# Kernel tuning notes

Hardware: AMD Instinct MI355X
Metric: run time of the kernel (lower is better)

## Reference

```python
import jax, jax.numpy as jnp
import numpy as np

N = 20000      # nodes
E = 320000     # edges (avg degree 16)
F_IN = 32      # raw node feature dim
D = 128        # GNN_EMBEDDING_DIM = out_channels per head
HEADS = 4
RNN_H = 128    # RNN_HIDDEN_DIM
NEG_SLOPE = 0.2


def setup_inputs() -> dict:
    key = jax.random.key(0)
    ks = jax.random.split(key, 16)
    s = 0.05
    return {
        "node_features": jax.random.normal(ks[0], (N, F_IN), jnp.float32),
        "hidden_state": jax.random.normal(ks[1], (1, RNN_H), jnp.float32),
        "W_enc": jax.random.normal(ks[2], (F_IN, D), jnp.float32) * s,
        "b_enc": jax.random.normal(ks[3], (D,), jnp.float32) * s,
        "W_l": jax.random.normal(ks[4], (D, HEADS * D), jnp.float32) * s,
        "b_l": jax.random.normal(ks[5], (HEADS * D,), jnp.float32) * s,
        "W_r": jax.random.normal(ks[6], (D, HEADS * D), jnp.float32) * s,
        "b_r": jax.random.normal(ks[7], (HEADS * D,), jnp.float32) * s,
        "att": jax.random.normal(ks[8], (HEADS, D), jnp.float32) * s,
        "gat_bias": jax.random.normal(ks[9], (D,), jnp.float32) * s,
        "W_ih": jax.random.normal(ks[10], (3 * RNN_H, D), jnp.float32) * s,
        "W_hh": jax.random.normal(ks[11], (3 * RNN_H, RNN_H), jnp.float32) * s,
        "b_ih": jax.random.normal(ks[12], (3 * RNN_H,), jnp.float32) * s,
        "b_hh": jax.random.normal(ks[13], (3 * RNN_H,), jnp.float32) * s,
        "edge_index": jax.random.randint(ks[14], (2, E), 0, N, jnp.int32),
    }


def reference(node_features, hidden_state, W_enc, b_enc, W_l, b_l, W_r, b_r,
              att, gat_bias, W_ih, W_hh, b_ih, b_hh, edge_index):
    n = node_features.shape[0]
    # node encoder + ReLU
    h = jax.nn.relu(node_features @ W_enc + b_enc)                 # [N, D]

    # GATv2Conv (heads=4, concat=False), add_self_loops=True, eval (no dropout)
    loop = jnp.arange(n, dtype=edge_index.dtype)
    src = jnp.concatenate([edge_index[0], loop])                   # source j
    dst = jnp.concatenate([edge_index[1], loop])                   # target i

    xl = (h @ W_l + b_l).reshape(n, HEADS, D)                      # source proj
    xr = (h @ W_r + b_r).reshape(n, HEADS, D)                      # target proj

    e = jax.nn.leaky_relu(xl[src] + xr[dst], NEG_SLOPE)            # [Et, H, C]
    logits = jnp.einsum('ehc,hc->eh', e, att)                      # [Et, H]

    # segment softmax over incoming edges of each target node
    m = jax.ops.segment_max(logits, dst, num_segments=n)           # [N, H]
    m = jnp.where(jnp.isfinite(m), m, 0.0)
    p = jnp.exp(logits - m[dst])
    denom = jax.ops.segment_sum(p, dst, num_segments=n)
    alpha = p / jnp.maximum(denom[dst], 1e-16)                     # [Et, H]

    out = jax.ops.segment_sum(xl[src] * alpha[..., None], dst, num_segments=n)
    gat = out.mean(axis=1) + gat_bias                              # [N, D]

    # agent node 0 -> GRUCell (torch gate order: r, z, n)
    x = gat[0:1]                                                   # [1, D]
    gi = x @ W_ih.T + b_ih
    gh = hidden_state @ W_hh.T + b_hh
    i_r, i_z, i_n = jnp.split(gi, 3, axis=-1)
    h_r, h_z, h_n = jnp.split(gh, 3, axis=-1)
    r = jax.nn.sigmoid(i_r + h_r)
    z = jax.nn.sigmoid(i_z + h_z)
    ng = jnp.tanh(i_n + r * h_n)
    return (1.0 - z) * ng + z * hidden_state                       # [1, RNN_H]
```

## Files before the change

kernel.cpp:

```cpp
#include <hip/hip_runtime.h>


#define NBLK 28
#define NXL  16
#define NGT  12
#define NCH  11
#define SLOTS3 8
#define CAP  40
#define FLAGMAGIC 0x5A5A0000u

struct KP {
    const int* ei; int E;
    const float *nf, *W_enc, *b_enc, *W_l, *b_l, *W_r, *b_r, *att, *gat_bias,
                *hprev, *W_ih, *W_hh, *b_ih, *b_hh;
    unsigned *scnt;
    unsigned *xlflag;
    unsigned *o0flag;
    int      *sslots;
    float *lgpart;
    float *out0;
    float *out;
};

__device__ __forceinline__ unsigned pollFlag(unsigned* p) {
    for (long it = 0; it < 50000000L; ++it) {
        unsigned v = atomicOr(p, 0u);
        if ((v & 0xFFFF0000u) == FLAGMAGIC) return v & 0xFFFFu;
        __builtin_amdgcn_s_sleep(2);
    }
    return 0u;
}

__device__ __forceinline__ float sigm(float x) { return 1.f / (1.f + expf(-x)); }

__global__ __launch_bounds__(256) void k_all(KP p)
{
    __shared__ __align__(16) float buf[14720];
    __shared__ float aux[512];
    __shared__ int   iaux[128];
    const int t = threadIdx.x, b = blockIdx.x;

    if (t == 0) iaux[0] = 0;
    __syncthreads();
    if ((p.E & 3) == 0) {
        int nv = p.E >> 2;
        int per = (nv + NBLK - 1) / NBLK;
        int lo = b * per, hi = min(lo + per, nv);
        const int4* d4 = (const int4*)(p.ei + p.E);
        for (int base = lo; base < hi; base += 256 * 12) {
            int4 v[12];
            #pragma unroll
            for (int k = 0; k < 12; ++k) {
                int i = base + t + k * 256;
                v[k] = (i < hi) ? d4[i] : make_int4(1, 1, 1, 1);
            }
            #pragma unroll
            for (int k = 0; k < 12; ++k) {
                int i = base + t + k * 256;
                if (v[k].x == 0 || v[k].y == 0 || v[k].z == 0 || v[k].w == 0) {
                    #pragma unroll
                    for (int c = 0; c < 4; ++c) {
                        if ((&v[k].x)[c] == 0) {
                            int q = atomicAdd(&iaux[0], 1);
                            if (q < SLOTS3) iaux[8 + q] = p.ei[4 * (long)i + c];
                        }
                    }
                }
            }
        }
    } else {
        int per = (p.E + NBLK - 1) / NBLK;
        long lo = (long)b * per, hi = lo + per; if (hi > p.E) hi = p.E;
        for (long i = lo + t; i < hi; i += 256) {
            if (p.ei[p.E + i] == 0) {
                int q = atomicAdd(&iaux[0], 1);
                if (q < SLOTS3) iaux[8 + q] = p.ei[i];
            }
        }
    }
    __syncthreads();
    int myc = min(iaux[0], SLOTS3);
    if (t < myc) p.sslots[b * SLOTS3 + t] = iaux[8 + t];
    __syncthreads();
    __threadfence();
    if (t == 0) atomicExch(&p.scnt[b * 16], FLAGMAGIC | (unsigned)myc);

    if (b < NXL) {
        const int l5 = t & 31, hw = t >> 5;
        const int j = b * 32 + l5;
        float blv = p.b_l[j], atv = p.att[j];
        float brv = (t < 32) ? p.b_r[b * 32 + t] : 0.f;
        for (int idx = t; idx < 1024; idx += 256) {
            int row = idx >> 3, f4 = idx & 7;
            ((float4*)buf)[idx] = *(const float4*)(p.W_l + (long)row * 512 + b * 32 + f4 * 4);
        }
        for (int idx = t; idx < 1024; idx += 256)
            ((float4*)(buf + 4096))[idx] = ((const float4*)p.W_enc)[idx];

        if (t < NBLK) iaux[32 + t] = (int)pollFlag(&p.scnt[t * 16]);
        __syncthreads();
        __threadfence();
        if (t < 64) {
            int c = (t < NBLK) ? iaux[32 + t] : 0;
            int pre = c;
            #pragma unroll
            for (int off = 1; off < 64; off <<= 1) {
                int v = __shfl_up(pre, off);
                if (t >= off) pre += v;
            }
            int base = pre - c;
            for (int u = 0; u < c; ++u) {
                int pos = base + u;
                if (pos < CAP - 1) iaux[64 + pos] = p.sslots[t * SLOTS3 + u];
            }
            if (t == 63) iaux[1] = min(pre, CAP - 1);
        }
        __syncthreads();
        int Mc = iaux[1];
        if (t == 0) iaux[64 + Mc] = 0;
        __syncthreads();
        int Mt = Mc + 1;

        for (int idx = t; idx < Mt * 8; idx += 256) {
            int e = idx >> 3, f4 = idx & 7;
            ((float4*)(buf + 8192))[idx] = *(const float4*)(p.nf + (long)iaux[64 + e] * 32 + f4 * 4);
        }
        __syncthreads();
        {
            int eg = t >> 7, c = t & 127;
            for (int e = eg; e < Mt; e += 2) {
                float a0 = 0, a1 = 0, a2 = 0, a3 = 0;
                #pragma unroll
                for (int k = 0; k < 32; k += 4) {
                    a0 += buf[8192 + e * 32 + k]     * buf[4096 + k * 128 + c];
                    a1 += buf[8192 + e * 32 + k + 1] * buf[4096 + (k + 1) * 128 + c];
                    a2 += buf[8192 + e * 32 + k + 2] * buf[4096 + (k + 2) * 128 + c];
                    a3 += buf[8192 + e * 32 + k + 3] * buf[4096 + (k + 3) * 128 + c];
                }
                buf[9600 + e * 128 + c] = fmaxf(a0 + a1 + a2 + a3 + p.b_enc[c], 0.f);
            }
        }
        __syncthreads();
        for (int idx = t; idx < 1024; idx += 256) {
            int row = idx >> 3, f4 = idx & 7;
            ((float4*)(buf + 4096))[idx] = *(const float4*)(p.W_r + (long)row * 512 + b * 32 + f4 * 4);
        }
        __syncthreads();
        if (t < 32) {
            float s0 = 0, s1 = 0, s2 = 0, s3 = 0;
            const float* h0 = &buf[9600 + (Mt - 1) * 128];
            #pragma unroll 8
            for (int c = 0; c < 128; c += 4) {
                s0 += h0[c]     * buf[4096 + c * 32 + t];
                s1 += h0[c + 1] * buf[4096 + (c + 1) * 32 + t];
                s2 += h0[c + 2] * buf[4096 + (c + 2) * 32 + t];
                s3 += h0[c + 3] * buf[4096 + (c + 3) * 32 + t];
            }
            aux[192 + t] = s0 + s1 + s2 + s3 + brv;
        }
        int ne = 0, el[5] = {0, 0, 0, 0, 0};
        for (int e = hw; e < Mt; e += 8) el[ne++] = e;
        float acc[5] = {0, 0, 0, 0, 0};
        #pragma unroll 4
        for (int c = 0; c < 128; c += 4) {
            float w0 = buf[c * 32 + l5],       w1 = buf[(c + 1) * 32 + l5];
            float w2 = buf[(c + 2) * 32 + l5], w3 = buf[(c + 3) * 32 + l5];
            #pragma unroll
            for (int k = 0; k < 5; ++k) {
                if (k < ne) {
                    float4 h4 = *(const float4*)&buf[9600 + el[k] * 128 + c];
                    acc[k] += h4.x * w0 + h4.y * w1 + h4.z * w2 + h4.w * w3;
                }
            }
        }
        __syncthreads();
        {
            float xrj = aux[192 + l5];
            #pragma unroll
            for (int k = 0; k < 5; ++k) {
                if (k < ne) {
                    int e = el[k];
                    float xv = acc[k] + blv;
                    buf[8192 + e * 32 + l5] = xv;
                    float v = xv + xrj;
                    v = (v > 0.f) ? v : 0.2f * v;
                    float pp = v * atv;
                    #pragma unroll
                    for (int off = 16; off; off >>= 1) pp += __shfl_down(pp, off, 32);
                    if (l5 == 0) aux[e] = pp;
                }
            }
        }
        __syncthreads();
        if (t < Mt) p.lgpart[b * CAP + t] = aux[t];
        __syncthreads();
        __threadfence();
        if (t == 0) atomicExch(&p.xlflag[b * 16], FLAGMAGIC | 1u);

        if (t < NXL) pollFlag(&p.xlflag[t * 16]);
        __syncthreads();
        __threadfence();
        for (int idx = t; idx < NXL * CAP; idx += 256)
            buf[idx] = p.lgpart[idx];
        __syncthreads();
        if (t < 4) {
            int h = t;
            float m = -1e30f;
            for (int e = 0; e < Mt; ++e) {
                float lv = buf[(4 * h) * CAP + e] + buf[(4 * h + 1) * CAP + e]
                         + buf[(4 * h + 2) * CAP + e] + buf[(4 * h + 3) * CAP + e];
                aux[256 + e * 4 + h] = lv;
                m = fmaxf(m, lv);
            }
            float d = 0.f;
            for (int e = 0; e < Mt; ++e) d += expf(aux[256 + e * 4 + h] - m);
            float inv = 1.f / fmaxf(d, 1e-16f);
            for (int e = 0; e < Mt; ++e)
                aux[256 + e * 4 + h] = expf(aux[256 + e * 4 + h] - m) * inv;
        }
        __syncthreads();
        if (t < 32) {
            int h = b >> 2;
            float s = 0.f;
            for (int e = 0; e < Mt; ++e)
                s += aux[256 + e * 4 + h] * buf[8192 + e * 32 + t];
            p.out0[b * 32 + t] = s;
        }
        __syncthreads();
        __threadfence();
        if (t == 0) atomicExch(&p.o0flag[b * 16], FLAGMAGIC | 1u);
        return;
    }

    {
        int g = b - NXL;
        int nch = min(NCH, 128 - g * NCH);
        if (t < 128) aux[256 + t] = p.hprev[t];
        for (int idx = t; idx < 6 * NCH * 32; idx += 256) {
            int chunk = idx / (NCH * 32);
            int rin = (idx % (NCH * 32)) >> 5;
            int f4 = idx & 31;
            if (rin < nch) {
                int grow = (chunk % 3) * 128 + g * NCH + rin;
                const float* W = (chunk < 3) ? p.W_ih : p.W_hh;
                ((float4*)buf)[idx] = *(const float4*)(W + (long)grow * 128 + f4 * 4);
            }
        }
        __syncthreads();
        {
            int w = t >> 6, l = t & 63;
            for (int rr = w; rr < 3 * nch; rr += 4) {
                int gate = rr / nch, rin = rr % nch;
                int chunk = 3 + gate;
                float2 wv = ((const float2*)&buf[chunk * (NCH * 128) + rin * 128])[l];
                float pp = wv.x * aux[256 + 2 * l] + wv.y * aux[256 + 2 * l + 1];
                #pragma unroll
                for (int off = 32; off; off >>= 1) pp += __shfl_down(pp, off);
                if (l == 0) aux[rr] = pp + p.b_hh[gate * 128 + g * NCH + rin];
            }
        }
        if (t < NXL) pollFlag(&p.o0flag[t * 16]);
        __syncthreads();
        __threadfence();
        if (t < 128)
            aux[384 + t] = 0.25f * (p.out0[t] + p.out0[128 + t] +
                                    p.out0[256 + t] + p.out0[384 + t])
                         + p.gat_bias[t];
        __syncthreads();
        {
            int w = t >> 6, l = t & 63;
            for (int rr = w; rr < 3 * nch; rr += 4) {
                int gate = rr / nch, rin = rr % nch;
                float2 wv = ((const float2*)&buf[gate * (NCH * 128) + rin * 128])[l];
                float pp = wv.x * aux[384 + 2 * l] + wv.y * aux[384 + 2 * l + 1];
                #pragma unroll
                for (int off = 32; off; off >>= 1) pp += __shfl_down(pp, off);
                if (l == 0) aux[64 + rr] = pp + p.b_ih[gate * 128 + g * NCH + rin];
            }
        }
        __syncthreads();
        if (t < nch) {
            int c = g * NCH + t;
            float r = sigm(aux[64 + t]           + aux[t]);
            float z = sigm(aux[64 + nch + t]     + aux[nch + t]);
            float n = tanhf(aux[64 + 2 * nch + t] + r * aux[2 * nch + t]);
            p.out[c] = (1.f - z) * n + z * aux[256 + c];
        }
    }
}

extern "C" void kernel_launch(void* const* d_in, const int* in_sizes, int n_in,
                              void* d_out, int out_size, void* d_ws, size_t ws_size,
                              hipStream_t stream) {
    KP kp;
    kp.nf       = (const float*)d_in[0];
    kp.hprev    = (const float*)d_in[1];
    kp.W_enc    = (const float*)d_in[2];
    kp.b_enc    = (const float*)d_in[3];
    kp.W_l      = (const float*)d_in[4];
    kp.b_l      = (const float*)d_in[5];
    kp.W_r      = (const float*)d_in[6];
    kp.b_r      = (const float*)d_in[7];
    kp.att      = (const float*)d_in[8];
    kp.gat_bias = (const float*)d_in[9];
    kp.W_ih     = (const float*)d_in[10];
    kp.W_hh     = (const float*)d_in[11];
    kp.b_ih     = (const float*)d_in[12];
    kp.b_hh     = (const float*)d_in[13];
    kp.ei       = (const int*)d_in[14];
    kp.E = in_sizes[14] / 2;

    char* ws = (char*)d_ws;
    kp.scnt   = (unsigned*)(ws + 0);
    kp.xlflag = (unsigned*)(ws + 1792);
    kp.o0flag = (unsigned*)(ws + 2816);
    kp.sslots = (int*)(ws + 3840);
    kp.lgpart = (float*)(ws + 4736);
    kp.out0   = (float*)(ws + 7296);
    kp.out    = (float*)d_out;

    k_all<<<NBLK, 256, 0, stream>>>(kp);
}
```

Measured before the change: 114.3 us.

## Merge GAT and GRU roles into 16 uniform blocks with overlapped weight loads

Reduces the grid from 28 blocks split into 16 GAT blocks and 12 GRU blocks to 16 blocks that each do both roles. Each block now computes its GAT slice and then 8 rows per gate of the GRU. While waiting on the cross-block logit flag, each block loads its W_ih and W_hh rows and computes the hidden-state matvec, and biases are prefetched at kernel start. This removes the separate GRU blocks' wait on the GAT blocks. In exchange each block does more serial work, and the edge scan for node 0 is split across fewer blocks.

Result: slower. 118.8 us (+4.0%).

```diff
diff --git a/kernel.cpp b/kernel.cpp
--- a/kernel.cpp
+++ b/kernel.cpp
@@ -1,11 +1,8 @@
 #include <hip/hip_runtime.h>
 
 
-#define NBLK 28
-#define NXL  16
-#define NGT  12
-#define NCH  11
-#define SLOTS3 8
+#define NBLK 16
+#define SLOTS3 12
 #define CAP  40
 #define FLAGMAGIC 0x5A5A0000u
 
@@ -33,12 +30,24 @@
 
 __device__ __forceinline__ float sigm(float x) { return 1.f / (1.f + expf(-x)); }
 
+
 __global__ __launch_bounds__(256) void k_all(KP p)
 {
     __shared__ __align__(16) float buf[14720];
-    __shared__ float aux[512];
+    __shared__ float aux[576];
     __shared__ int   iaux[128];
     const int t = threadIdx.x, b = blockIdx.x;
+    const int l5 = t & 31, hw = t >> 5;
+    const int j = b * 32 + l5;
+
+    float blv = p.b_l[j], atv = p.att[j];
+    float brv = (t < 32) ? p.b_r[b * 32 + t] : 0.f;
+    if (t < 128) { aux[224 + t] = p.hprev[t]; aux[352 + t] = p.gat_bias[t]; }
+    if (t >= 128 && t < 152) {
+        int rr = t - 128, gate = rr >> 3, rin = rr & 7;
+        aux[528 + rr] = p.b_ih[gate * 128 + b * 8 + rin];
+        aux[552 + rr] = p.b_hh[gate * 128 + b * 8 + rin];
+    }
 
     if (t == 0) iaux[0] = 0;
     __syncthreads();
@@ -85,207 +94,192 @@
     __threadfence();
     if (t == 0) atomicExch(&p.scnt[b * 16], FLAGMAGIC | (unsigned)myc);
 
-    if (b < NXL) {
-        const int l5 = t & 31, hw = t >> 5;
-        const int j = b * 32 + l5;
-        float blv = p.b_l[j], atv = p.att[j];
-        float brv = (t < 32) ? p.b_r[b * 32 + t] : 0.f;
-        for (int idx = t; idx < 1024; idx += 256) {
-            int row = idx >> 3, f4 = idx & 7;
-            ((float4*)buf)[idx] = *(const float4*)(p.W_l + (long)row * 512 + b * 32 + f4 * 4);
-        }
-        for (int idx = t; idx < 1024; idx += 256)
-            ((float4*)(buf + 4096))[idx] = ((const float4*)p.W_enc)[idx];
-
-        if (t < NBLK) iaux[32 + t] = (int)pollFlag(&p.scnt[t * 16]);
-        __syncthreads();
-        __threadfence();
-        if (t < 64) {
-            int c = (t < NBLK) ? iaux[32 + t] : 0;
-            int pre = c;
-            #pragma unroll
-            for (int off = 1; off < 64; off <<= 1) {
-                int v = __shfl_up(pre, off);
-                if (t >= off) pre += v;
-            }
-            int base = pre - c;
-            for (int u = 0; u < c; ++u) {
-                int pos = base + u;
-                if (pos < CAP - 1) iaux[64 + pos] = p.sslots[t * SLOTS3 + u];
-            }
-            if (t == 63) iaux[1] = min(pre, CAP - 1);
-        }
-        __syncthreads();
-        int Mc = iaux[1];
-        if (t == 0) iaux[64 + Mc] = 0;
-        __syncthreads();
-        int Mt = Mc + 1;
-
-        for (int idx = t; idx < Mt * 8; idx += 256) {
-            int e = idx >> 3, f4 = idx & 7;
-            ((float4*)(buf + 8192))[idx] = *(const float4*)(p.nf + (long)iaux[64 + e] * 32 + f4 * 4);
-        }
-        __syncthreads();
-        {
-            int eg = t >> 7, c = t & 127;
-            for (int e = eg; e < Mt; e += 2) {
-                float a0 = 0, a1 = 0, a2 = 0, a3 = 0;
+    for (int idx = t; idx < 1024; idx += 256) {
+        int row = idx >> 3, f4 = idx & 7;
+        ((float4*)buf)[idx] = *(const float4*)(p.W_l + (long)row * 512 + b * 32 + f4 * 4);
+    }
+    for (int idx = t; idx < 1024; idx += 256)
+        ((float4*)(buf + 4096))[idx] = ((const float4*)p.W_enc)[idx];
+
+    if (t < NBLK) iaux[32 + t] = (int)pollFlag(&p.scnt[t * 16]);
+    __syncthreads();
+    __threadfence();
+    if (t < 64) {
+        int c = (t < NBLK) ? iaux[32 + t] : 0;
+        int pre = c;
+        #pragma unroll
+        for (int off = 1; off < 64; off <<= 1) {
+            int v = __shfl_up(pre, off);
+            if (t >= off) pre += v;
+        }
+        int base = pre - c;
+        for (int u = 0; u < c; ++u) {
+            int pos = base + u;
+            if (pos < CAP - 1) iaux[64 + pos] = p.sslots[t * SLOTS3 + u];
+        }
+        if (t == 63) iaux[1] = min(pre, CAP - 1);
+    }
+    __syncthreads();
+    int Mc = iaux[1];
+    if (t == 0) iaux[64 + Mc] = 0;
+    __syncthreads();
+    int Mt = Mc + 1;
+
+    for (int idx = t; idx < Mt * 8; idx += 256) {
+        int e = idx >> 3, f4 = idx & 7;
+        ((float4*)(buf + 8192))[idx] = *(const float4*)(p.nf + (long)iaux[64 + e] * 32 + f4 * 4);
+    }
+    __syncthreads();
+    {
+        int eg = t >> 7, c = t & 127;
+        for (int e = eg; e < Mt; e += 2) {
+            float a0 = 0, a1 = 0, a2 = 0, a3 = 0;
+            #pragma unroll
+            for (int k = 0; k < 32; k += 4) {
+                a0 += buf[8192 + e * 32 + k]     * buf[4096 + k * 128 + c];
+                a1 += buf[8192 + e * 32 + k + 1] * buf[4096 + (k + 1) * 128 + c];
+                a2 += buf[8192 + e * 32 + k + 2] * buf[4096 + (k + 2) * 128 + c];
+                a3 += buf[8192 + e * 32 + k + 3] * buf[4096 + (k + 3) * 128 + c];
+            }
+            buf[9472 + e * 128 + c] = fmaxf(a0 + a1 + a2 + a3 + p.b_enc[c], 0.f);
+        }
+    }
+    __syncthreads();
+    for (int idx = t; idx < 1024; idx += 256) {
+        int row = idx >> 3, f4 = idx & 7;
+        ((float4*)(buf + 4096))[idx] = *(const float4*)(p.W_r + (long)row * 512 + b * 32 + f4 * 4);
+    }
+    __syncthreads();
+    if (t < 32) {
+        float s0 = 0, s1 = 0, s2 = 0, s3 = 0;
+        const float* h0 = &buf[9472 + (Mt - 1) * 128];
+        #pragma unroll 8
+        for (int c = 0; c < 128; c += 4) {
+            s0 += h0[c]     * buf[4096 + c * 32 + t];
+            s1 += h0[c + 1] * buf[4096 + (c + 1) * 32 + t];
+            s2 += h0[c + 2] * buf[4096 + (c + 2) * 32 + t];
+            s3 += h0[c + 3] * buf[4096 + (c + 3) * 32 + t];
+        }
+        aux[192 + t] = s0 + s1 + s2 + s3 + brv;
+    }
+    int ne = 0, el[5] = {0, 0, 0, 0, 0};
+    for (int e = hw; e < Mt; e += 8) el[ne++] = e;
+    float acc[5] = {0, 0, 0, 0, 0};
+    #pragma unroll 4
+    for (int c = 0; c < 128; c += 4) {
+        float w0 = buf[c * 32 + l5],       w1 = buf[(c + 1) * 32 + l5];
+        float w2 = buf[(c + 2) * 32 + l5], w3 = buf[(c + 3) * 32 + l5];
+        #pragma unroll
+        for (int k = 0; k < 5; ++k) {
+            if (k < ne) {
+                float4 h4 = *(const float4*)&buf[9472 + el[k] * 128 + c];
+                acc[k] += h4.x * w0 + h4.y * w1 + h4.z * w2 + h4.w * w3;
+            }
+        }
+    }
+    __syncthreads();
+    {
+        float xrj = aux[192 + l5];
+        #pragma unroll
+        for (int k = 0; k < 5; ++k) {
+            if (k < ne) {
+                int e = el[k];
+                float xv = acc[k] + blv;
+                buf[8192 + e * 32 + l5] = xv;
+                float v = xv + xrj;
+                v = (v > 0.f) ? v : 0.2f * v;
+                float pp = v * atv;
                 #pragma unroll
-                for (int k = 0; k < 32; k += 4) {
-                    a0 += buf[8192 + e * 32 + k]     * buf[4096 + k * 128 + c];
-                    a1 += buf[8192 + e * 32 + k + 1] * buf[4096 + (k + 1) * 128 + c];
-                    a2 += buf[8192 + e * 32 + k + 2] * buf[4096 + (k + 2) * 128 + c];
-                    a3 += buf[8192 + e * 32 + k + 3] * buf[4096 + (k + 3) * 128 + c];
-                }
-                buf[9600 + e * 128 + c] = fmaxf(a0 + a1 + a2 + a3 + p.b_enc[c], 0.f);
-            }
-        }
-        __syncthreads();
-        for (int idx = t; idx < 1024; idx += 256) {
-            int row = idx >> 3, f4 = idx & 7;
-            ((float4*)(buf + 4096))[idx] = *(const float4*)(p.W_r + (long)row * 512 + b * 32 + f4 * 4);
-        }
-        __syncthreads();
-        if (t < 32) {
-            float s0 = 0, s1 = 0, s2 = 0, s3 = 0;
-            const float* h0 = &buf[9600 + (Mt - 1) * 128];
-            #pragma unroll 8
-            for (int c = 0; c < 128; c += 4) {
-                s0 += h0[c]     * buf[4096 + c * 32 + t];
-                s1 += h0[c + 1] * buf[4096 + (c + 1) * 32 + t];
-                s2 += h0[c + 2] * buf[4096 + (c + 2) * 32 + t];
-                s3 += h0[c + 3] * buf[4096 + (c + 3) * 32 + t];
-            }
-            aux[192 + t] = s0 + s1 + s2 + s3 + brv;
-        }
-        int ne = 0, el[5] = {0, 0, 0, 0, 0};
-        for (int e = hw; e < Mt; e += 8) el[ne++] = e;
-        float acc[5] = {0, 0, 0, 0, 0};
-        #pragma unroll 4
-        for (int c = 0; c < 128; c += 4) {
-            float w0 = buf[c * 32 + l5],       w1 = buf[(c + 1) * 32 + l5];
-            float w2 = buf[(c + 2) * 32 + l5], w3 = buf[(c + 3) * 32 + l5];
-            #pragma unroll
-            for (int k = 0; k < 5; ++k) {
-                if (k < ne) {
-                    float4 h4 = *(const float4*)&buf[9600 + el[k] * 128 + c];
-                    acc[k] += h4.x * w0 + h4.y * w1 + h4.z * w2 + h4.w * w3;
-                }
-            }
-        }
-        __syncthreads();
-        {
-            float xrj = aux[192 + l5];
-            #pragma unroll
-            for (int k = 0; k < 5; ++k) {
-                if (k < ne) {
-                    int e = el[k];
-                    float xv = acc[k] + blv;
-                    buf[8192 + e * 32 + l5] = xv;
-                    float v = xv + xrj;
-                    v = (v > 0.f) ? v : 0.2f * v;
-                    float pp = v * atv;
-                    #pragma unroll
-                    for (int off = 16; off; off >>= 1) pp += __shfl_down(pp, off, 32);
-                    if (l5 == 0) aux[e] = pp;
-                }
-            }
-        }
-        __syncthreads();
-        if (t < Mt) p.lgpart[b * CAP + t] = aux[t];
-        __syncthreads();
-        __threadfence();
-        if (t == 0) atomicExch(&p.xlflag[b * 16], FLAGMAGIC | 1u);
-
-        if (t < NXL) pollFlag(&p.xlflag[t * 16]);
-        __syncthreads();
-        __threadfence();
-        for (int idx = t; idx < NXL * CAP; idx += 256)
-            buf[idx] = p.lgpart[idx];
-        __syncthreads();
-        if (t < 4) {
-            int h = t;
-            float m = -1e30f;
-            for (int e = 0; e < Mt; ++e) {
-                float lv = buf[(4 * h) * CAP + e] + buf[(4 * h + 1) * CAP + e]
-                         + buf[(4 * h + 2) * CAP + e] + buf[(4 * h + 3) * CAP + e];
-                aux[256 + e * 4 + h] = lv;
-                m = fmaxf(m, lv);
-            }
-            float d = 0.f;
-            for (int e = 0; e < Mt; ++e) d += expf(aux[256 + e * 4 + h] - m);
-            float inv = 1.f / fmaxf(d, 1e-16f);
-            for (int e = 0; e < Mt; ++e)
-                aux[256 + e * 4 + h] = expf(aux[256 + e * 4 + h] - m) * inv;
-        }
-        __syncthreads();
-        if (t < 32) {
-            int h = b >> 2;
-            float s = 0.f;
-            for (int e = 0; e < Mt; ++e)
-                s += aux[256 + e * 4 + h] * buf[8192 + e * 32 + t];
-            p.out0[b * 32 + t] = s;
-        }
-        __syncthreads();
-        __threadfence();
-        if (t == 0) atomicExch(&p.o0flag[b * 16], FLAGMAGIC | 1u);
-        return;
-    }
-
+                for (int off = 16; off; off >>= 1) pp += __shfl_down(pp, off, 32);
+                if (l5 == 0) aux[e] = pp;
+            }
+        }
+    }
+    __syncthreads();
+    if (t < Mt) p.lgpart[b * CAP + t] = aux[t];
+    __syncthreads();
+    __threadfence();
+    if (t == 0) atomicExch(&p.xlflag[b * 16], FLAGMAGIC | 1u);
+
+    for (int idx = t; idx < 768; idx += 256) {
+        int rr = idx >> 5, f4 = idx & 31;
+        int grow = (rr >> 3) * 128 + b * 8 + (rr & 7);
+        ((float4*)buf)[idx] = *(const float4*)(p.W_ih + (long)grow * 128 + f4 * 4);
+        ((float4*)(buf + 3072))[idx] = *(const float4*)(p.W_hh + (long)grow * 128 + f4 * 4);
+    }
+    __syncthreads();
     {
-        int g = b - NXL;
-        int nch = min(NCH, 128 - g * NCH);
-        if (t < 128) aux[256 + t] = p.hprev[t];
-        for (int idx = t; idx < 6 * NCH * 32; idx += 256) {
-            int chunk = idx / (NCH * 32);
-            int rin = (idx % (NCH * 32)) >> 5;
-            int f4 = idx & 31;
-            if (rin < nch) {
-                int grow = (chunk % 3) * 128 + g * NCH + rin;
-                const float* W = (chunk < 3) ? p.W_ih : p.W_hh;
-                ((float4*)buf)[idx] = *(const float4*)(W + (long)grow * 128 + f4 * 4);
-            }
-        }
-        __syncthreads();
-        {
-            int w = t >> 6, l = t & 63;
-            for (int rr = w; rr < 3 * nch; rr += 4) {
-                int gate = rr / nch, rin = rr % nch;
-                int chunk = 3 + gate;
-                float2 wv = ((const float2*)&buf[chunk * (NCH * 128) + rin * 128])[l];
-                float pp = wv.x * aux[256 + 2 * l] + wv.y * aux[256 + 2 * l + 1];
-                #pragma unroll
-                for (int off = 32; off; off >>= 1) pp += __shfl_down(pp, off);
-                if (l == 0) aux[rr] = pp + p.b_hh[gate * 128 + g * NCH + rin];
-            }
-        }
-        if (t < NXL) pollFlag(&p.o0flag[t * 16]);
-        __syncthreads();
-        __threadfence();
-        if (t < 128)
-            aux[384 + t] = 0.25f * (p.out0[t] + p.out0[128 + t] +
-                                    p.out0[256 + t] + p.out0[384 + t])
-                         + p.gat_bias[t];
-        __syncthreads();
-        {
-            int w = t >> 6, l = t & 63;
-            for (int rr = w; rr < 3 * nch; rr += 4) {
-                int gate = rr / nch, rin = rr % nch;
-                float2 wv = ((const float2*)&buf[gate * (NCH * 128) + rin * 128])[l];
-                float pp = wv.x * aux[384 + 2 * l] + wv.y * aux[384 + 2 * l + 1];
-                #pragma unroll
-                for (int off = 32; off; off >>= 1) pp += __shfl_down(pp, off);
-                if (l == 0) aux[64 + rr] = pp + p.b_ih[gate * 128 + g * NCH + rin];
-            }
-        }
-        __syncthreads();
-        if (t < nch) {
-            int c = g * NCH + t;
-            float r = sigm(aux[64 + t]           + aux[t]);
-            float z = sigm(aux[64 + nch + t]     + aux[nch + t]);
-            float n = tanhf(aux[64 + 2 * nch + t] + r * aux[2 * nch + t]);
-            p.out[c] = (1.f - z) * n + z * aux[256 + c];
-        }
+        int w = t >> 6, l = t & 63;
+        #pragma unroll
+        for (int i = 0; i < 6; ++i) {
+            int rr = w * 6 + i;
+            float2 wv = ((const float2*)&buf[3072 + rr * 128])[l];
+            float pp = wv.x * aux[224 + 2 * l] + wv.y * aux[224 + 2 * l + 1];
+            #pragma unroll
+            for (int off = 32; off; off >>= 1) pp += __shfl_down(pp, off);
+            if (l == 0) aux[480 + rr] = pp + aux[552 + rr];
+        }
+    }
+
+    if (t < NBLK) pollFlag(&p.xlflag[t * 16]);
+    __syncthreads();
+    __threadfence();
+    for (int idx = t; idx < NBLK * CAP; idx += 256)
+        buf[6144 + idx] = p.lgpart[idx];
+    __syncthreads();
+    if (t < 4) {
+        int h = t;
+        float m = -1e30f;
+        for (int e = 0; e < Mt; ++e) {
+            float lv = buf[6144 + (4 * h) * CAP + e] + buf[6144 + (4 * h + 1) * CAP + e]
+                     + buf[6144 + (4 * h + 2) * CAP + e] + buf[6144 + (4 * h + 3) * CAP + e];
+            buf[6784 + e * 4 + h] = lv;
+            m = fmaxf(m, lv);
+        }
+        float d = 0.f;
+        for (int e = 0; e < Mt; ++e) d += expf(buf[6784 + e * 4 + h] - m);
+        float inv = 1.f / fmaxf(d, 1e-16f);
+        for (int e = 0; e < Mt; ++e)
+            buf[6784 + e * 4 + h] = expf(buf[6784 + e * 4 + h] - m) * inv;
+    }
+    __syncthreads();
+    if (t < 32) {
+        int h = b >> 2;
+        float s = 0.f;
+        for (int e = 0; e < Mt; ++e)
+            s += buf[6784 + e * 4 + h] * buf[8192 + e * 32 + t];
+        p.out0[b * 32 + t] = s;
+    }
+    __syncthreads();
+    __threadfence();
+    if (t == 0) atomicExch(&p.o0flag[b * 16], FLAGMAGIC | 1u);
+
+    if (t < NBLK) pollFlag(&p.o0flag[t * 16]);
+    __syncthreads();
+    __threadfence();
+    if (t < 128)
+        aux[64 + t] = 0.25f * (p.out0[t] + p.out0[128 + t] +
+                               p.out0[256 + t] + p.out0[384 + t]) + aux[352 + t];
+    __syncthreads();
+    {
+        int w = t >> 6, l = t & 63;
+        #pragma unroll
+        for (int i = 0; i < 6; ++i) {
+            int rr = w * 6 + i;
+            float2 wv = ((const float2*)&buf[rr * 128])[l];
+            float pp = wv.x * aux[64 + 2 * l] + wv.y * aux[64 + 2 * l + 1];
+            #pragma unroll
+            for (int off = 32; off; off >>= 1) pp += __shfl_down(pp, off);
+            if (l == 0) aux[504 + rr] = pp + aux[528 + rr];
+        }
+    }
+    __syncthreads();
+    if (t < 8) {
+        int c = b * 8 + t;
+        float r = sigm(aux[504 + t]      + aux[480 + t]);
+        float z = sigm(aux[504 + 8 + t]  + aux[480 + 8 + t]);
+        float n = tanhf(aux[504 + 16 + t] + r * aux[480 + 16 + t]);
+        p.out[c] = (1.f - z) * n + z * aux[224 + c];
     }
 }
 
@@ -312,11 +306,11 @@
 
     char* ws = (char*)d_ws;
     kp.scnt   = (unsigned*)(ws + 0);
-    kp.xlflag = (unsigned*)(ws + 1792);
-    kp.o0flag = (unsigned*)(ws + 2816);
-    kp.sslots = (int*)(ws + 3840);
-    kp.lgpart = (float*)(ws + 4736);
-    kp.out0   = (float*)(ws + 7296);
+    kp.xlflag = (unsigned*)(ws + 1024);
+    kp.o0flag = (unsigned*)(ws + 2048);
+    kp.sslots = (int*)(ws + 3072);
+    kp.lgpart = (float*)(ws + 3840);
+    kp.out0   = (float*)(ws + 6400);
     kp.out    = (float*)d_out;
 
     k_all<<<NBLK, 256, 0, stream>>>(kp);
```
